# Kernel optimization log

Hardware: AMD Instinct MI355X
Metric: run time of the kernel (lower is better)

Reference implementation:

```python
import jax, jax.numpy as jnp
import numpy as np

B, S, DM1, DM2, DK, DV = 8, 2048, 768, 768, 64, 64
EPS = 1e-5


def setup_inputs() -> dict:
    key = jax.random.key(0)
    ks = jax.random.split(key, 8)
    s1 = 1.0 / np.sqrt(DM1)
    s2 = 1.0 / np.sqrt(DM2)
    return {
        "x_1": jax.random.normal(ks[0], (B, S, DM1), jnp.float32),
        "x_2": jax.random.normal(ks[1], (B, S, DM2), jnp.float32),
        "Wq": jax.random.uniform(ks[2], (DM1, DK), jnp.float32, -s1, s1),
        "bq": jnp.zeros((DK,), jnp.float32),
        "Wk": jax.random.uniform(ks[3], (DM2, DK), jnp.float32, -s2, s2),
        "bk": jnp.zeros((DK,), jnp.float32),
        "Wv": jax.random.uniform(ks[4], (DM2, DV), jnp.float32, -s2, s2),
        "bv": jnp.zeros((DV,), jnp.float32),
        "gamma": jnp.ones((DV,), jnp.float32),
        "beta": jnp.zeros((DV,), jnp.float32),
    }


def reference(x_1, x_2, Wq, bq, Wk, bk, Wv, bv, gamma, beta):
    q = jnp.einsum("bsd,dk->bsk", x_1, Wq) + bq            # [B,S,DK]
    k = jnp.einsum("bsd,dk->bsk", x_2, Wk) + bk            # [B,S,DK]
    v = jnp.einsum("bsd,dv->bsv", x_2, Wv) + bv            # [B,S,DV]
    scores = jnp.einsum("bqk,bsk->bqs", q, k) / jnp.sqrt(jnp.float32(DK))
    w = jax.nn.softmax(scores, axis=-1)                    # [B,S,S]
    # reverse-weight transform (reverse=True)
    dim = w.shape[1]
    w = (1.0 - w) / (dim - 1)
    attn = jnp.einsum("bqs,bsv->bqv", w, v)                # [B,S,DV]
    mu = jnp.mean(attn, axis=-1, keepdims=True)
    var = jnp.var(attn, axis=-1, keepdims=True)
    out = (attn - mu) * jax.lax.rsqrt(var + EPS) * gamma + beta
    return out
```

## Files before the change

kernel.cpp:

```cpp
#include <hip/hip_runtime.h>
#include <hip/hip_bf16.h>

#define BATCH 8
#define SEQ   2048
#define DM    768
#define DD    64
#define BS (BATCH * SEQ)
#define SCALEQ 0.1803369380478f

typedef __bf16 bf16x8 __attribute__((ext_vector_type(8)));
typedef float  f32x4  __attribute__((ext_vector_type(4)));
typedef short  short8 __attribute__((ext_vector_type(8)));
typedef short  short4v __attribute__((ext_vector_type(4)));

#define MFMA16(a, b, c) __builtin_amdgcn_mfma_f32_16x16x32_bf16((a), (b), (c), 0, 0, 0)

__device__ __forceinline__ short f2bf(float x) {
    unsigned u = __builtin_bit_cast(unsigned, x);
    u = (u + 0x7fffu + ((u >> 16) & 1u)) >> 16;
    return (short)u;
}
__device__ __forceinline__ float bf2f(short s) {
    unsigned u = ((unsigned)(unsigned short)s) << 16;
    return __builtin_bit_cast(float, u);
}
__device__ __forceinline__ bf16x8 cvt8v(f32x4 a, f32x4 b) {
    bf16x8 r;
    r[0] = (__bf16)a[0]; r[1] = (__bf16)a[1]; r[2] = (__bf16)a[2]; r[3] = (__bf16)a[3];
    r[4] = (__bf16)b[0]; r[5] = (__bf16)b[1]; r[6] = (__bf16)b[2]; r[7] = (__bf16)b[3];
    return r;
}
__device__ __forceinline__ void glds16(const void* g, void* l) {
    __builtin_amdgcn_global_load_lds(
        (const __attribute__((address_space(1))) void*)g,
        (__attribute__((address_space(3))) void*)l, 16, 0, 0);
}

__global__ void prep_w_kernel(const float* __restrict__ Wq, const float* __restrict__ Wk,
                              const float* __restrict__ Wv, short* __restrict__ Wt) {
    int idx = blockIdx.x * 256 + threadIdx.x;
    if (idx >= 3 * DM * DD) return;
    int m = idx / (DM * DD);
    int r = (idx % (DM * DD)) / DD;
    int c = idx % DD;
    const float* W = (m == 0) ? Wq : (m == 1) ? Wk : Wv;
    float scale = (m == 0) ? SCALEQ : 1.0f;
    Wt[m * DM * DD + c * DM + r] = f2bf(W[r * DD + c] * scale);
}

__global__ __launch_bounds__(256) void proj_kernel(
        const float* __restrict__ x1, const float* __restrict__ x2,
        const short* __restrict__ Wt,
        const float* __restrict__ bq, const float* __restrict__ bk,
        const float* __restrict__ bv,
        short* __restrict__ Qs, short* __restrict__ Kb, short* __restrict__ Vtb,
        float* __restrict__ C) {
    __shared__ __align__(16) float xl[2][64 * 64];
    __shared__ __align__(16) short wl[2][2][64 * 64];
    const int tid = threadIdx.x, wave = tid >> 6, lane = tid & 63;
    const int quad = lane >> 4, l15 = lane & 15;
    const int kv = blockIdx.x >> 8;
    const int r0 = (blockIdx.x & 255) * 64;
    const float* x = kv ? x2 : x1;
    const short* W0 = Wt + (kv ? (size_t)(DM * DD) : 0);
    const short* W1 = Wt + 2 * (size_t)(DM * DD);

    const int xri = lane >> 4, xsl = lane & 15;
    const int wri = lane >> 3, wsl = lane & 7;

    f32x4 acc0[4] = {}, acc1[4] = {};

    {
#pragma unroll
        for (int j = 0; j < 4; j++) {
            int rl = wave * 16 + j * 4 + xri;
            int piece = xsl ^ (rl & 7);
            glds16(x + (size_t)(r0 + rl) * DM + piece * 4, &xl[0][(wave * 16 + j * 4) * 64]);
        }
#pragma unroll
        for (int t = 0; t < 2; t++) {
            int rl = wave * 16 + t * 8 + wri;
            int piece = wsl ^ (rl & 7);
            glds16(W0 + (size_t)rl * DM + piece * 8, &wl[0][0][(wave * 16 + t * 8) * 64]);
            if (kv)
                glds16(W1 + (size_t)rl * DM + piece * 8, &wl[0][1][(wave * 16 + t * 8) * 64]);
        }
    }
    __syncthreads();

    const int sw = l15 & 7;
    const int arow = (wave * 16 + l15) * 64;
    for (int it = 0; it < 12; it++) {
        const int buf = it & 1;
        if (it < 11) {
            const int k0 = (it + 1) * 64;
#pragma unroll
            for (int j = 0; j < 4; j++) {
                int rl = wave * 16 + j * 4 + xri;
                int piece = xsl ^ (rl & 7);
                glds16(x + (size_t)(r0 + rl) * DM + k0 + piece * 4,
                       &xl[buf ^ 1][(wave * 16 + j * 4) * 64]);
            }
#pragma unroll
            for (int t = 0; t < 2; t++) {
                int rl = wave * 16 + t * 8 + wri;
                int piece = wsl ^ (rl & 7);
                glds16(W0 + (size_t)rl * DM + k0 + piece * 8,
                       &wl[buf ^ 1][0][(wave * 16 + t * 8) * 64]);
                if (kv)
                    glds16(W1 + (size_t)rl * DM + k0 + piece * 8,
                           &wl[buf ^ 1][1][(wave * 16 + t * 8) * 64]);
            }
        }
#pragma unroll
        for (int kc = 0; kc < 2; kc++) {
            f32x4 a0 = *(const f32x4*)&xl[buf][arow + ((kc * 8 + quad * 2) ^ sw) * 4];
            f32x4 a1 = *(const f32x4*)&xl[buf][arow + ((kc * 8 + quad * 2 + 1) ^ sw) * 4];
            bf16x8 af = cvt8v(a0, a1);
#pragma unroll
            for (int tn = 0; tn < 4; tn++) {
                bf16x8 b0 = *(const bf16x8*)&wl[buf][0][(tn * 16 + l15) * 64 + ((kc * 4 + quad) ^ sw) * 8];
                acc0[tn] = MFMA16(af, b0, acc0[tn]);
                if (kv) {
                    bf16x8 b1 = *(const bf16x8*)&wl[buf][1][(tn * 16 + l15) * 64 + ((kc * 4 + quad) ^ sw) * 8];
                    acc1[tn] = MFMA16(af, b1, acc1[tn]);
                }
            }
        }
        __syncthreads();
    }

    if (!kv) {
#pragma unroll
        for (int tn = 0; tn < 4; tn++) {
            int v = tn * 16 + l15;
            float bb = bq[v] * SCALEQ;
#pragma unroll
            for (int r = 0; r < 4; r++)
                Qs[(size_t)(r0 + wave * 16 + quad * 4 + r) * DD + v] = f2bf(acc0[tn][r] + bb);
        }
    } else {
#pragma unroll
        for (int tn = 0; tn < 4; tn++) {
            int v = tn * 16 + l15;
            float bb = bk[v];
#pragma unroll
            for (int r = 0; r < 4; r++)
                Kb[(size_t)(r0 + wave * 16 + quad * 4 + r) * DD + v] = f2bf(acc0[tn][r] + bb);
        }
        const int b = r0 / SEQ;
        const int sbase = (r0 % SEQ) + wave * 16 + quad * 4;
#pragma unroll
        for (int tn = 0; tn < 4; tn++) {
            int v = tn * 16 + l15;
            float bb = bv[v];
            short4v pk;
            float cs = 0.f;
#pragma unroll
            for (int r = 0; r < 4; r++) {
                pk[r] = f2bf(acc1[tn][r] + bb);
                cs += bf2f(pk[r]);
            }
            *(short4v*)(Vtb + ((size_t)b * DD + v) * SEQ + sbase) = pk;
            cs += __shfl_xor(cs, 16);
            cs += __shfl_xor(cs, 32);
            if (quad == 0) atomicAdd(&C[b * DD + v], cs);
        }
    }
}

#define PBS 72
__global__ __launch_bounds__(256, 2) void flash_kernel(
        const short* __restrict__ Q, const short* __restrict__ K,
        const short* __restrict__ Vt,
        short* __restrict__ Yp, float* __restrict__ Dp) {
    __shared__ __align__(16) short pbuf[4][64 * PBS];
    __shared__ float dl[4][64];
    const int tid  = threadIdx.x;
    const int wave = tid >> 6, lane = tid & 63, quad = lane >> 4, l15 = lane & 15;
    const int blk = blockIdx.x;
    const int b = blk & 7, qt = (blk >> 3) & 31, half = blk >> 8;
    const int q0 = qt * 64;

    bf16x8 qf[4][2];
#pragma unroll
    for (int qn = 0; qn < 4; qn++)
#pragma unroll
        for (int kc = 0; kc < 2; kc++)
            qf[qn][kc] = *(const bf16x8*)(Q + ((size_t)(b * SEQ + q0 + qn * 16 + l15)) * DD + kc * 32 + quad * 8);

    const short* Kbp = K  + (size_t)b * SEQ * DD;
    const short* Vbp = Vt + (size_t)b * DD * SEQ;
    f32x4 y[4][4] = {};
    float den[4] = {0.f, 0.f, 0.f, 0.f};
    short* pw = &pbuf[wave][0];

    const int s_begin = half * 1024 + wave * 256;
    for (int s0 = s_begin; s0 < s_begin + 256; s0 += 64) {
#pragma unroll
        for (int tn = 0; tn < 4; tn++) {
            const short* kf = Kbp + (size_t)(s0 + tn * 16 + l15) * DD + quad * 8;
            bf16x8 ka0 = *(const bf16x8*)kf;
            bf16x8 ka1 = *(const bf16x8*)(kf + 32);
#pragma unroll
            for (int qn = 0; qn < 4; qn++) {
                f32x4 z = {0.f, 0.f, 0.f, 0.f};
                z = MFMA16(ka0, qf[qn][0], z);
                z = MFMA16(ka1, qf[qn][1], z);
                short4v pk;
#pragma unroll
                for (int r = 0; r < 4; r++) {
                    float p = __builtin_amdgcn_exp2f(z[r]);
                    den[qn] += p;
                    pk[r] = f2bf(p);
                }
                *(short4v*)&pw[(qn * 16 + l15) * PBS + tn * 16 + quad * 4] = pk;
            }
        }
#pragma unroll
        for (int kc = 0; kc < 2; kc++) {
            bf16x8 pB[4];
#pragma unroll
            for (int qn = 0; qn < 4; qn++)
                pB[qn] = *(const bf16x8*)&pw[(qn * 16 + l15) * PBS + kc * 32 + quad * 8];
#pragma unroll
            for (int vn = 0; vn < 4; vn++) {
                bf16x8 va = *(const bf16x8*)(Vbp + (size_t)(vn * 16 + l15) * SEQ + s0 + kc * 32 + quad * 8);
#pragma unroll
                for (int qn = 0; qn < 4; qn++)
                    y[qn][vn] = MFMA16(va, pB[qn], y[qn][vn]);
            }
        }
    }
#pragma unroll
    for (int qn = 0; qn < 4; qn++) {
        den[qn] += __shfl_xor(den[qn], 16);
        den[qn] += __shfl_xor(den[qn], 32);
    }
#pragma unroll
    for (int qn = 0; qn < 4; qn++) {
#pragma unroll
        for (int vn = 0; vn < 4; vn++) {
            short4v pk;
#pragma unroll
            for (int r = 0; r < 4; r++) pk[r] = f2bf(y[qn][vn][r]);
            *(short4v*)&pw[(qn * 16 + l15) * PBS + vn * 16 + quad * 4] = pk;
        }
        if (quad == 0) dl[wave][qn * 16 + l15] = den[qn];
    }
    __syncthreads();
    {
        const int q = wave * 16 + l15;
        float D = dl[0][q] + dl[1][q] + dl[2][q] + dl[3][q];
        float ys[16];
#pragma unroll
        for (int j = 0; j < 16; j++) ys[j] = 0.f;
#pragma unroll
        for (int u = 0; u < 4; u++) {
#pragma unroll
            for (int h = 0; h < 2; h++) {
                bf16x8 t = *(const bf16x8*)&pbuf[u][q * PBS + quad * 16 + h * 8];
#pragma unroll
                for (int j = 0; j < 8; j++) ys[h * 8 + j] += (float)t[j];
            }
        }
        const size_t row = (size_t)b * SEQ + q0 + q;
        short8 o0, o1;
#pragma unroll
        for (int j = 0; j < 8; j++) { o0[j] = f2bf(ys[j]); o1[j] = f2bf(ys[8 + j]); }
        short* yout = Yp + ((size_t)half * BS + row) * DD + quad * 16;
        *(short8*)yout = o0;
        *(short8*)(yout + 8) = o1;
        if (quad == 0) Dp[half * BS + row] = D;
    }
}

__global__ __launch_bounds__(256) void reduce_ln_kernel(
        const short* __restrict__ Yp, const float* __restrict__ Dp,
        const float* __restrict__ C, const float* __restrict__ gamma,
        const float* __restrict__ beta, float* __restrict__ out) {
    const int row = blockIdx.x * 4 + (threadIdx.x >> 6);
    const int v = threadIdx.x & 63;
    const int b = row >> 11;
    float Y = bf2f(Yp[(size_t)row * DD + v]) + bf2f(Yp[((size_t)BS + row) * DD + v]);
    float D = Dp[row] + Dp[BS + row];
    float attn = (C[b * DD + v] - Y / D) * (1.0f / (float)(SEQ - 1));
    float msum = attn, ssum = attn * attn;
#pragma unroll
    for (int m = 1; m < 64; m <<= 1) {
        msum += __shfl_xor(msum, m);
        ssum += __shfl_xor(ssum, m);
    }
    float mu = msum * (1.0f / 64.0f);
    float var = ssum * (1.0f / 64.0f) - mu * mu;
    float rs = rsqrtf(var + 1e-5f);
    out[(size_t)row * DD + v] = (attn - mu) * rs * gamma[v] + beta[v];
}

extern "C" void kernel_launch(void* const* d_in, const int* in_sizes, int n_in,
                              void* d_out, int out_size, void* d_ws, size_t ws_size,
                              hipStream_t stream) {
    const float* x1    = (const float*)d_in[0];
    const float* x2    = (const float*)d_in[1];
    const float* Wq    = (const float*)d_in[2];
    const float* bq    = (const float*)d_in[3];
    const float* Wk    = (const float*)d_in[4];
    const float* bk    = (const float*)d_in[5];
    const float* Wv    = (const float*)d_in[6];
    const float* bv    = (const float*)d_in[7];
    const float* gamma = (const float*)d_in[8];
    const float* beta  = (const float*)d_in[9];
    float* out = (float*)d_out;

    char* ws = (char*)d_ws;
    short* Qs  = (short*)(ws);
    short* Kbf = (short*)(ws + (2ull << 20));
    short* Vtb = (short*)(ws + (4ull << 20));
    short* Wt  = (short*)(ws + (6ull << 20));
    float* Cc  = (float*)(ws + (6ull << 20) + 3 * DM * DD * 2);
    short* Yp  = (short*)(ws + (7ull << 20));
    float* Dp  = (float*)(ws + (11ull << 20));

    hipMemsetAsync(Cc, 0, BATCH * DD * sizeof(float), stream);
    prep_w_kernel<<<576, 256, 0, stream>>>(Wq, Wk, Wv, Wt);
    proj_kernel<<<512, 256, 0, stream>>>(x1, x2, Wt, bq, bk, bv, Qs, Kbf, Vtb, Cc);
    flash_kernel<<<512, 256, 0, stream>>>(Qs, Kbf, Vtb, Yp, Dp);
    reduce_ln_kernel<<<BS / 4, 256, 0, stream>>>(Yp, Dp, Cc, gamma, beta, out);
}
```

Baseline: 173.1 us.

## Fuse LayerNorm into flash kernel, drop split-S halves and W LDS staging

The flash kernel now handles 32 query rows over the full key range per block instead of 64 rows over half the keys. That removes the Yp/Dp partial buffers and the separate reduce_ln kernel, and the LayerNorm is done in the flash epilogue. The hipMemset of C is folded into prep_w_kernel. The projection kernel stops staging the weight tiles in LDS and reads them straight from global memory, trusting the cache. Each block now does twice as many key iterations with fewer query rows, so K/V reuse per block is lower, and the direct weight loads may add latency.

New measurement: 218.6 us. +26.3%, slower.

```diff
diff --git a/kernel.cpp b/kernel.cpp
--- a/kernel.cpp
+++ b/kernel.cpp
@@ -37,8 +37,10 @@
 }
 
 __global__ void prep_w_kernel(const float* __restrict__ Wq, const float* __restrict__ Wk,
-                              const float* __restrict__ Wv, short* __restrict__ Wt) {
+                              const float* __restrict__ Wv, short* __restrict__ Wt,
+                              float* __restrict__ C) {
     int idx = blockIdx.x * 256 + threadIdx.x;
+    if (idx < BATCH * DD) C[idx] = 0.f;
     if (idx >= 3 * DM * DD) return;
     int m = idx / (DM * DD);
     int r = (idx % (DM * DD)) / DD;
@@ -56,7 +58,6 @@
         short* __restrict__ Qs, short* __restrict__ Kb, short* __restrict__ Vtb,
         float* __restrict__ C) {
     __shared__ __align__(16) float xl[2][64 * 64];
-    __shared__ __align__(16) short wl[2][2][64 * 64];
     const int tid = threadIdx.x, wave = tid >> 6, lane = tid & 63;
     const int quad = lane >> 4, l15 = lane & 15;
     const int kv = blockIdx.x >> 8;
@@ -66,25 +67,14 @@
     const short* W1 = Wt + 2 * (size_t)(DM * DD);
 
     const int xri = lane >> 4, xsl = lane & 15;
-    const int wri = lane >> 3, wsl = lane & 7;
 
     f32x4 acc0[4] = {}, acc1[4] = {};
 
-    {
-#pragma unroll
-        for (int j = 0; j < 4; j++) {
-            int rl = wave * 16 + j * 4 + xri;
-            int piece = xsl ^ (rl & 7);
-            glds16(x + (size_t)(r0 + rl) * DM + piece * 4, &xl[0][(wave * 16 + j * 4) * 64]);
-        }
-#pragma unroll
-        for (int t = 0; t < 2; t++) {
-            int rl = wave * 16 + t * 8 + wri;
-            int piece = wsl ^ (rl & 7);
-            glds16(W0 + (size_t)rl * DM + piece * 8, &wl[0][0][(wave * 16 + t * 8) * 64]);
-            if (kv)
-                glds16(W1 + (size_t)rl * DM + piece * 8, &wl[0][1][(wave * 16 + t * 8) * 64]);
-        }
+#pragma unroll
+    for (int j = 0; j < 4; j++) {
+        int rl = wave * 16 + j * 4 + xri;
+        int piece = xsl ^ (rl & 7);
+        glds16(x + (size_t)(r0 + rl) * DM + piece * 4, &xl[0][(wave * 16 + j * 4) * 64]);
     }
     __syncthreads();
 
@@ -101,17 +91,8 @@
                 glds16(x + (size_t)(r0 + rl) * DM + k0 + piece * 4,
                        &xl[buf ^ 1][(wave * 16 + j * 4) * 64]);
             }
-#pragma unroll
-            for (int t = 0; t < 2; t++) {
-                int rl = wave * 16 + t * 8 + wri;
-                int piece = wsl ^ (rl & 7);
-                glds16(W0 + (size_t)rl * DM + k0 + piece * 8,
-                       &wl[buf ^ 1][0][(wave * 16 + t * 8) * 64]);
-                if (kv)
-                    glds16(W1 + (size_t)rl * DM + k0 + piece * 8,
-                           &wl[buf ^ 1][1][(wave * 16 + t * 8) * 64]);
-            }
-        }
+        }
+        const int kbase = it * 64;
 #pragma unroll
         for (int kc = 0; kc < 2; kc++) {
             f32x4 a0 = *(const f32x4*)&xl[buf][arow + ((kc * 8 + quad * 2) ^ sw) * 4];
@@ -119,10 +100,12 @@
             bf16x8 af = cvt8v(a0, a1);
 #pragma unroll
             for (int tn = 0; tn < 4; tn++) {
-                bf16x8 b0 = *(const bf16x8*)&wl[buf][0][(tn * 16 + l15) * 64 + ((kc * 4 + quad) ^ sw) * 8];
+                bf16x8 b0 = *(const bf16x8*)(W0 + (size_t)(tn * 16 + l15) * DM
+                                             + kbase + kc * 32 + quad * 8);
                 acc0[tn] = MFMA16(af, b0, acc0[tn]);
                 if (kv) {
-                    bf16x8 b1 = *(const bf16x8*)&wl[buf][1][(tn * 16 + l15) * 64 + ((kc * 4 + quad) ^ sw) * 8];
+                    bf16x8 b1 = *(const bf16x8*)(W1 + (size_t)(tn * 16 + l15) * DM
+                                                 + kbase + kc * 32 + quad * 8);
                     acc1[tn] = MFMA16(af, b1, acc1[tn]);
                 }
             }
@@ -170,40 +153,42 @@
 }
 
 #define PBS 72
-__global__ __launch_bounds__(256, 2) void flash_kernel(
+__global__ __launch_bounds__(256) void flash_kernel(
         const short* __restrict__ Q, const short* __restrict__ K,
-        const short* __restrict__ Vt,
-        short* __restrict__ Yp, float* __restrict__ Dp) {
-    __shared__ __align__(16) short pbuf[4][64 * PBS];
-    __shared__ float dl[4][64];
+        const short* __restrict__ Vt, const float* __restrict__ C,
+        const float* __restrict__ gamma, const float* __restrict__ beta,
+        float* __restrict__ out) {
+    __shared__ __align__(16) short pbuf[4][32 * PBS];
+    __shared__ float dl[4][32];
     const int tid  = threadIdx.x;
     const int wave = tid >> 6, lane = tid & 63, quad = lane >> 4, l15 = lane & 15;
     const int blk = blockIdx.x;
-    const int b = blk & 7, qt = (blk >> 3) & 31, half = blk >> 8;
-    const int q0 = qt * 64;
-
-    bf16x8 qf[4][2];
-#pragma unroll
-    for (int qn = 0; qn < 4; qn++)
+    const int b = blk & 7, qt = blk >> 3;
+    const int q0 = qt * 32;
+
+    bf16x8 qf[2][2];
+#pragma unroll
+    for (int qn = 0; qn < 2; qn++)
 #pragma unroll
         for (int kc = 0; kc < 2; kc++)
-            qf[qn][kc] = *(const bf16x8*)(Q + ((size_t)(b * SEQ + q0 + qn * 16 + l15)) * DD + kc * 32 + quad * 8);
+            qf[qn][kc] = *(const bf16x8*)(Q + ((size_t)(b * SEQ + q0 + qn * 16 + l15)) * DD
+                                          + kc * 32 + quad * 8);
 
     const short* Kbp = K  + (size_t)b * SEQ * DD;
     const short* Vbp = Vt + (size_t)b * DD * SEQ;
-    f32x4 y[4][4] = {};
-    float den[4] = {0.f, 0.f, 0.f, 0.f};
+    f32x4 y[2][4] = {};
+    float den[2] = {0.f, 0.f};
     short* pw = &pbuf[wave][0];
 
-    const int s_begin = half * 1024 + wave * 256;
-    for (int s0 = s_begin; s0 < s_begin + 256; s0 += 64) {
+    const int s_begin = wave * 512;
+    for (int s0 = s_begin; s0 < s_begin + 512; s0 += 64) {
 #pragma unroll
         for (int tn = 0; tn < 4; tn++) {
             const short* kf = Kbp + (size_t)(s0 + tn * 16 + l15) * DD + quad * 8;
             bf16x8 ka0 = *(const bf16x8*)kf;
             bf16x8 ka1 = *(const bf16x8*)(kf + 32);
 #pragma unroll
-            for (int qn = 0; qn < 4; qn++) {
+            for (int qn = 0; qn < 2; qn++) {
                 f32x4 z = {0.f, 0.f, 0.f, 0.f};
                 z = MFMA16(ka0, qf[qn][0], z);
                 z = MFMA16(ka1, qf[qn][1], z);
@@ -219,26 +204,27 @@
         }
 #pragma unroll
         for (int kc = 0; kc < 2; kc++) {
-            bf16x8 pB[4];
-#pragma unroll
-            for (int qn = 0; qn < 4; qn++)
+            bf16x8 pB[2];
+#pragma unroll
+            for (int qn = 0; qn < 2; qn++)
                 pB[qn] = *(const bf16x8*)&pw[(qn * 16 + l15) * PBS + kc * 32 + quad * 8];
 #pragma unroll
             for (int vn = 0; vn < 4; vn++) {
-                bf16x8 va = *(const bf16x8*)(Vbp + (size_t)(vn * 16 + l15) * SEQ + s0 + kc * 32 + quad * 8);
-#pragma unroll
-                for (int qn = 0; qn < 4; qn++)
+                bf16x8 va = *(const bf16x8*)(Vbp + (size_t)(vn * 16 + l15) * SEQ
+                                             + s0 + kc * 32 + quad * 8);
+#pragma unroll
+                for (int qn = 0; qn < 2; qn++)
                     y[qn][vn] = MFMA16(va, pB[qn], y[qn][vn]);
             }
         }
     }
 #pragma unroll
-    for (int qn = 0; qn < 4; qn++) {
+    for (int qn = 0; qn < 2; qn++) {
         den[qn] += __shfl_xor(den[qn], 16);
         den[qn] += __shfl_xor(den[qn], 32);
     }
 #pragma unroll
-    for (int qn = 0; qn < 4; qn++) {
+    for (int qn = 0; qn < 2; qn++) {
 #pragma unroll
         for (int vn = 0; vn < 4; vn++) {
             short4v pk;
@@ -250,51 +236,40 @@
     }
     __syncthreads();
     {
-        const int q = wave * 16 + l15;
+        const int q = tid >> 3;
+        const int v0 = (tid & 7) * 8;
         float D = dl[0][q] + dl[1][q] + dl[2][q] + dl[3][q];
-        float ys[16];
-#pragma unroll
-        for (int j = 0; j < 16; j++) ys[j] = 0.f;
+        float invD = 1.0f / D;
+        float ys[8];
+#pragma unroll
+        for (int j = 0; j < 8; j++) ys[j] = 0.f;
 #pragma unroll
         for (int u = 0; u < 4; u++) {
-#pragma unroll
-            for (int h = 0; h < 2; h++) {
-                bf16x8 t = *(const bf16x8*)&pbuf[u][q * PBS + quad * 16 + h * 8];
-#pragma unroll
-                for (int j = 0; j < 8; j++) ys[h * 8 + j] += (float)t[j];
-            }
-        }
+            bf16x8 t = *(const bf16x8*)&pbuf[u][q * PBS + v0];
+#pragma unroll
+            for (int j = 0; j < 8; j++) ys[j] += (float)t[j];
+        }
+        float attn[8], msum = 0.f, ssum = 0.f;
+#pragma unroll
+        for (int j = 0; j < 8; j++) {
+            float a = (C[b * DD + v0 + j] - ys[j] * invD) * (1.0f / (float)(SEQ - 1));
+            attn[j] = a;
+            msum += a;
+            ssum += a * a;
+        }
+#pragma unroll
+        for (int m = 1; m < 8; m <<= 1) {
+            msum += __shfl_xor(msum, m);
+            ssum += __shfl_xor(ssum, m);
+        }
+        float mu = msum * (1.0f / 64.0f);
+        float var = ssum * (1.0f / 64.0f) - mu * mu;
+        float rs = rsqrtf(var + 1e-5f);
         const size_t row = (size_t)b * SEQ + q0 + q;
-        short8 o0, o1;
-#pragma unroll
-        for (int j = 0; j < 8; j++) { o0[j] = f2bf(ys[j]); o1[j] = f2bf(ys[8 + j]); }
-        short* yout = Yp + ((size_t)half * BS + row) * DD + quad * 16;
-        *(short8*)yout = o0;
-        *(short8*)(yout + 8) = o1;
-        if (quad == 0) Dp[half * BS + row] = D;
-    }
-}
-
-__global__ __launch_bounds__(256) void reduce_ln_kernel(
-        const short* __restrict__ Yp, const float* __restrict__ Dp,
-        const float* __restrict__ C, const float* __restrict__ gamma,
-        const float* __restrict__ beta, float* __restrict__ out) {
-    const int row = blockIdx.x * 4 + (threadIdx.x >> 6);
-    const int v = threadIdx.x & 63;
-    const int b = row >> 11;
-    float Y = bf2f(Yp[(size_t)row * DD + v]) + bf2f(Yp[((size_t)BS + row) * DD + v]);
-    float D = Dp[row] + Dp[BS + row];
-    float attn = (C[b * DD + v] - Y / D) * (1.0f / (float)(SEQ - 1));
-    float msum = attn, ssum = attn * attn;
-#pragma unroll
-    for (int m = 1; m < 64; m <<= 1) {
-        msum += __shfl_xor(msum, m);
-        ssum += __shfl_xor(ssum, m);
-    }
-    float mu = msum * (1.0f / 64.0f);
-    float var = ssum * (1.0f / 64.0f) - mu * mu;
-    float rs = rsqrtf(var + 1e-5f);
-    out[(size_t)row * DD + v] = (attn - mu) * rs * gamma[v] + beta[v];
+#pragma unroll
+        for (int j = 0; j < 8; j++)
+            out[row * DD + v0 + j] = (attn[j] - mu) * rs * gamma[v0 + j] + beta[v0 + j];
+    }
 }
 
 extern "C" void kernel_launch(void* const* d_in, const int* in_sizes, int n_in,
@@ -318,12 +293,8 @@
     short* Vtb = (short*)(ws + (4ull << 20));
     short* Wt  = (short*)(ws + (6ull << 20));
     float* Cc  = (float*)(ws + (6ull << 20) + 3 * DM * DD * 2);
-    short* Yp  = (short*)(ws + (7ull << 20));
-    float* Dp  = (float*)(ws + (11ull << 20));
-
-    hipMemsetAsync(Cc, 0, BATCH * DD * sizeof(float), stream);
-    prep_w_kernel<<<576, 256, 0, stream>>>(Wq, Wk, Wv, Wt);
+
+    prep_w_kernel<<<576, 256, 0, stream>>>(Wq, Wk, Wv, Wt, Cc);
     proj_kernel<<<512, 256, 0, stream>>>(x1, x2, Wt, bq, bk, bv, Qs, Kbf, Vtb, Cc);
-    flash_kernel<<<512, 256, 0, stream>>>(Qs, Kbf, Vtb, Yp, Dp);
-    reduce_ln_kernel<<<BS / 4, 256, 0, stream>>>(Yp, Dp, Cc, gamma, beta, out);
-}
+    flash_kernel<<<512, 256, 0, stream>>>(Qs, Kbf, Vtb, Cc, gamma, beta, out);
+}
```

## Load projection activations directly into registers and fold memset into weight prep

Applied to the files above, without the earlier changes.

The projection kernel no longer stages the fp32 activation tile in shared memory. Each lane now loads its own fp32 fragment straight from global memory into registers, prefetching one K-step ahead, which cuts LDS traffic and shared memory footprint. Q and K/V blocks are also interleaved in the grid (kv = block & 1) so the heavier K/V blocks are spread out, and the separate hipMemsetAsync of the column-sum buffer is folded into prep_w_kernel to remove one launch. The tradeoff is higher register use and per-lane global loads that are less coalesced than the previous LDS-staged path.

New measurement: 171.5 us. Within noise of the previous version (-0.9%).

```diff
diff --git a/kernel.cpp b/kernel.cpp
--- a/kernel.cpp
+++ b/kernel.cpp
@@ -24,10 +24,10 @@
     unsigned u = ((unsigned)(unsigned short)s) << 16;
     return __builtin_bit_cast(float, u);
 }
-__device__ __forceinline__ bf16x8 cvt8v(f32x4 a, f32x4 b) {
+__device__ __forceinline__ bf16x8 cvt8(float4 a, float4 b) {
     bf16x8 r;
-    r[0] = (__bf16)a[0]; r[1] = (__bf16)a[1]; r[2] = (__bf16)a[2]; r[3] = (__bf16)a[3];
-    r[4] = (__bf16)b[0]; r[5] = (__bf16)b[1]; r[6] = (__bf16)b[2]; r[7] = (__bf16)b[3];
+    r[0] = (__bf16)a.x; r[1] = (__bf16)a.y; r[2] = (__bf16)a.z; r[3] = (__bf16)a.w;
+    r[4] = (__bf16)b.x; r[5] = (__bf16)b.y; r[6] = (__bf16)b.z; r[7] = (__bf16)b.w;
     return r;
 }
 __device__ __forceinline__ void glds16(const void* g, void* l) {
@@ -37,8 +37,10 @@
 }
 
 __global__ void prep_w_kernel(const float* __restrict__ Wq, const float* __restrict__ Wk,
-                              const float* __restrict__ Wv, short* __restrict__ Wt) {
+                              const float* __restrict__ Wv, short* __restrict__ Wt,
+                              float* __restrict__ C) {
     int idx = blockIdx.x * 256 + threadIdx.x;
+    if (idx < BATCH * DD) C[idx] = 0.f;
     if (idx >= 3 * DM * DD) return;
     int m = idx / (DM * DD);
     int r = (idx % (DM * DD)) / DD;
@@ -55,78 +57,71 @@
         const float* __restrict__ bv,
         short* __restrict__ Qs, short* __restrict__ Kb, short* __restrict__ Vtb,
         float* __restrict__ C) {
-    __shared__ __align__(16) float xl[2][64 * 64];
     __shared__ __align__(16) short wl[2][2][64 * 64];
     const int tid = threadIdx.x, wave = tid >> 6, lane = tid & 63;
     const int quad = lane >> 4, l15 = lane & 15;
-    const int kv = blockIdx.x >> 8;
-    const int r0 = (blockIdx.x & 255) * 64;
+    const int kv = blockIdx.x & 1;
+    const int r0 = (blockIdx.x >> 1) * 64;
     const float* x = kv ? x2 : x1;
     const short* W0 = Wt + (kv ? (size_t)(DM * DD) : 0);
     const short* W1 = Wt + 2 * (size_t)(DM * DD);
 
-    const int xri = lane >> 4, xsl = lane & 15;
-    const int wri = lane >> 3, wsl = lane & 7;
+    const int wrow = lane >> 3;
+    const int wpiece = ((lane & 7) ^ (lane >> 3)) * 8;
+
+    const float* xp = x + (size_t)(r0 + wave * 16 + l15) * DM + quad * 8;
 
     f32x4 acc0[4] = {}, acc1[4] = {};
 
-    {
-#pragma unroll
-        for (int j = 0; j < 4; j++) {
-            int rl = wave * 16 + j * 4 + xri;
-            int piece = xsl ^ (rl & 7);
-            glds16(x + (size_t)(r0 + rl) * DM + piece * 4, &xl[0][(wave * 16 + j * 4) * 64]);
-        }
-#pragma unroll
-        for (int t = 0; t < 2; t++) {
-            int rl = wave * 16 + t * 8 + wri;
-            int piece = wsl ^ (rl & 7);
-            glds16(W0 + (size_t)rl * DM + piece * 8, &wl[0][0][(wave * 16 + t * 8) * 64]);
-            if (kv)
-                glds16(W1 + (size_t)rl * DM + piece * 8, &wl[0][1][(wave * 16 + t * 8) * 64]);
-        }
-    }
+#pragma unroll
+    for (int j = 0; j < 2; j++) {
+        int rbase = wave * 16 + j * 8;
+        glds16(W0 + (size_t)(rbase + wrow) * DM + wpiece, &wl[0][0][rbase * 64]);
+        if (kv)
+            glds16(W1 + (size_t)(rbase + wrow) * DM + wpiece, &wl[0][1][rbase * 64]);
+    }
+    float4 c0a = *(const float4*)(xp);
+    float4 c0b = *(const float4*)(xp + 4);
+    float4 c1a = *(const float4*)(xp + 32);
+    float4 c1b = *(const float4*)(xp + 36);
     __syncthreads();
 
-    const int sw = l15 & 7;
-    const int arow = (wave * 16 + l15) * 64;
+    const int swz = l15 & 7;
+#pragma unroll
     for (int it = 0; it < 12; it++) {
         const int buf = it & 1;
+        float4 n0a, n0b, n1a, n1b;
         if (it < 11) {
             const int k0 = (it + 1) * 64;
 #pragma unroll
-            for (int j = 0; j < 4; j++) {
-                int rl = wave * 16 + j * 4 + xri;
-                int piece = xsl ^ (rl & 7);
-                glds16(x + (size_t)(r0 + rl) * DM + k0 + piece * 4,
-                       &xl[buf ^ 1][(wave * 16 + j * 4) * 64]);
-            }
-#pragma unroll
-            for (int t = 0; t < 2; t++) {
-                int rl = wave * 16 + t * 8 + wri;
-                int piece = wsl ^ (rl & 7);
-                glds16(W0 + (size_t)rl * DM + k0 + piece * 8,
-                       &wl[buf ^ 1][0][(wave * 16 + t * 8) * 64]);
+            for (int j = 0; j < 2; j++) {
+                int rbase = wave * 16 + j * 8;
+                glds16(W0 + (size_t)(rbase + wrow) * DM + k0 + wpiece,
+                       &wl[buf ^ 1][0][rbase * 64]);
                 if (kv)
-                    glds16(W1 + (size_t)rl * DM + k0 + piece * 8,
-                           &wl[buf ^ 1][1][(wave * 16 + t * 8) * 64]);
-            }
+                    glds16(W1 + (size_t)(rbase + wrow) * DM + k0 + wpiece,
+                           &wl[buf ^ 1][1][rbase * 64]);
+            }
+            n0a = *(const float4*)(xp + k0);
+            n0b = *(const float4*)(xp + k0 + 4);
+            n1a = *(const float4*)(xp + k0 + 32);
+            n1b = *(const float4*)(xp + k0 + 36);
         }
 #pragma unroll
         for (int kc = 0; kc < 2; kc++) {
-            f32x4 a0 = *(const f32x4*)&xl[buf][arow + ((kc * 8 + quad * 2) ^ sw) * 4];
-            f32x4 a1 = *(const f32x4*)&xl[buf][arow + ((kc * 8 + quad * 2 + 1) ^ sw) * 4];
-            bf16x8 af = cvt8v(a0, a1);
+            bf16x8 af = cvt8(kc ? c1a : c0a, kc ? c1b : c0b);
 #pragma unroll
             for (int tn = 0; tn < 4; tn++) {
-                bf16x8 b0 = *(const bf16x8*)&wl[buf][0][(tn * 16 + l15) * 64 + ((kc * 4 + quad) ^ sw) * 8];
+                const int slot = ((kc * 4 + quad) ^ swz) * 8;
+                bf16x8 b0 = *(const bf16x8*)&wl[buf][0][(tn * 16 + l15) * 64 + slot];
                 acc0[tn] = MFMA16(af, b0, acc0[tn]);
                 if (kv) {
-                    bf16x8 b1 = *(const bf16x8*)&wl[buf][1][(tn * 16 + l15) * 64 + ((kc * 4 + quad) ^ sw) * 8];
+                    bf16x8 b1 = *(const bf16x8*)&wl[buf][1][(tn * 16 + l15) * 64 + slot];
                     acc1[tn] = MFMA16(af, b1, acc1[tn]);
                 }
             }
         }
+        c0a = n0a; c0b = n0b; c1a = n1a; c1b = n1b;
         __syncthreads();
     }
 
@@ -187,7 +182,8 @@
     for (int qn = 0; qn < 4; qn++)
 #pragma unroll
         for (int kc = 0; kc < 2; kc++)
-            qf[qn][kc] = *(const bf16x8*)(Q + ((size_t)(b * SEQ + q0 + qn * 16 + l15)) * DD + kc * 32 + quad * 8);
+            qf[qn][kc] = *(const bf16x8*)(Q + ((size_t)(b * SEQ + q0 + qn * 16 + l15)) * DD
+                                          + kc * 32 + quad * 8);
 
     const short* Kbp = K  + (size_t)b * SEQ * DD;
     const short* Vbp = Vt + (size_t)b * DD * SEQ;
@@ -225,7 +221,8 @@
                 pB[qn] = *(const bf16x8*)&pw[(qn * 16 + l15) * PBS + kc * 32 + quad * 8];
 #pragma unroll
             for (int vn = 0; vn < 4; vn++) {
-                bf16x8 va = *(const bf16x8*)(Vbp + (size_t)(vn * 16 + l15) * SEQ + s0 + kc * 32 + quad * 8);
+                bf16x8 va = *(const bf16x8*)(Vbp + (size_t)(vn * 16 + l15) * SEQ
+                                             + s0 + kc * 32 + quad * 8);
 #pragma unroll
                 for (int qn = 0; qn < 4; qn++)
                     y[qn][vn] = MFMA16(va, pB[qn], y[qn][vn]);
@@ -321,8 +318,7 @@
     short* Yp  = (short*)(ws + (7ull << 20));
     float* Dp  = (float*)(ws + (11ull << 20));
 
-    hipMemsetAsync(Cc, 0, BATCH * DD * sizeof(float), stream);
-    prep_w_kernel<<<576, 256, 0, stream>>>(Wq, Wk, Wv, Wt);
+    prep_w_kernel<<<576, 256, 0, stream>>>(Wq, Wk, Wv, Wt, Cc);
     proj_kernel<<<512, 256, 0, stream>>>(x1, x2, Wt, bq, bk, bv, Qs, Kbf, Vtb, Cc);
     flash_kernel<<<512, 256, 0, stream>>>(Qs, Kbf, Vtb, Yp, Dp);
     reduce_ln_kernel<<<BS / 4, 256, 0, stream>>>(Yp, Dp, Cc, gamma, beta, out);
```
